# Performance work log

Measured on AMD Instinct MI355X. Metric: run time of the kernel, lower is better.

Reference implementation:

```python
import jax, jax.numpy as jnp
import numpy as np

N, E, B = 100000, 1600000, 128
ND, ED, H, NC = 91, 20, 128, 3
EPS = 1e-5


def setup_inputs() -> dict:
    key = jax.random.key(0)
    ks = jax.random.split(key, 16)
    s = 0.05
    inp = {
        "node_feats": jax.random.normal(ks[0], (N, ND), jnp.float32),
        "edge_index": jax.random.randint(ks[1], (2, E), 0, N, dtype=jnp.int32),
        "edge_feats": jax.random.normal(ks[2], (E, ED), jnp.float32),
        "batch": jnp.sort(jax.random.randint(ks[3], (N,), 0, B, dtype=jnp.int32)),
        # params
        "embed_w": jax.random.normal(ks[4], (ND, H), jnp.float32) * s,
        "embed_b": jnp.zeros((H,), jnp.float32),
        "conv_wsrc": jax.random.normal(ks[5], (NC, H, 2 * H), jnp.float32) * s,
        "conv_wdst": jax.random.normal(ks[6], (NC, H, 2 * H), jnp.float32) * s,
        "conv_we": jax.random.normal(ks[7], (NC, ED, 2 * H), jnp.float32) * s,
        "conv_b": jnp.zeros((NC, 2 * H), jnp.float32),
        "bn_gamma": jnp.ones((NC, H), jnp.float32),
        "bn_beta": jnp.zeros((NC, H), jnp.float32),
        "fc1_w": jax.random.normal(ks[8], (H, H), jnp.float32) * s,
        "fc1_b": jnp.zeros((H,), jnp.float32),
        "fc_bn_gamma": jnp.ones((H,), jnp.float32),
        "fc_bn_beta": jnp.zeros((H,), jnp.float32),
        "out_w": jax.random.normal(ks[9], (H, 1), jnp.float32) * s,
        "out_b": jnp.zeros((1,), jnp.float32),
    }
    return inp


def _bn(x, gamma, beta):
    # training-mode batchnorm over axis 0, biased variance (torch semantics)
    m = x.mean(0)
    v = x.var(0)
    return (x - m) * jax.lax.rsqrt(v + EPS) * gamma + beta


def reference(node_feats, edge_index, edge_feats, batch, embed_w, embed_b,
              conv_wsrc, conv_wdst, conv_we, conv_b, bn_gamma, bn_beta,
              fc1_w, fc1_b, fc_bn_gamma, fc_bn_beta, out_w, out_b):
    h = node_feats @ embed_w + embed_b  # (N, H)
    src, dst = edge_index[0], edge_index[1]
    for i in range(NC):
        # CGCNN gated conv: Linear on concat[h_src, h_dst, e] split into 3 matmuls
        z = (h[src] @ conv_wsrc[i] + h[dst] @ conv_wdst[i]
             + edge_feats @ conv_we[i] + conv_b[i])  # (E, 2H)
        msg = jax.nn.sigmoid(z[:, :H]) * jax.nn.softplus(z[:, H:])
        agg = jax.ops.segment_sum(msg, dst, num_segments=N)  # (N, H)
        h = jax.nn.relu(h + _bn(agg, bn_gamma[i], bn_beta[i]))
    # global mean pool over graphs
    counts = jnp.maximum(
        jax.ops.segment_sum(jnp.ones((h.shape[0], 1), h.dtype), batch, num_segments=B), 1.0)
    g = jax.ops.segment_sum(h, batch, num_segments=B) / counts  # (B, H)
    x = jax.nn.relu(_bn(g @ fc1_w + fc1_b, fc_bn_gamma, fc_bn_beta))
    return x @ out_w + out_b  # (B, 1)
```

## Files before the change

kernel.cpp:

```cpp
#include <hip/hip_runtime.h>
#include <hip/hip_bf16.h>

#define NN 100000
#define EE 1600000
#define HH 128
#define NDIM 91
#define EDIM 20
#define BB 128
#define EPSF 1e-5f
#define NBLK 4096
#define PER 400
#define ECAP (NBLK * PER)
#define LN2I 1.44269504f
#define NPART 512

typedef __attribute__((ext_vector_type(8))) short short8v;
typedef __attribute__((ext_vector_type(4))) float f32x4;

__device__ __forceinline__ short f2bs(float x) {
  __hip_bfloat16 b = __float2bfloat16(x);
  return *reinterpret_cast<short*>(&b);
}
__device__ __forceinline__ float bl(unsigned int u) {
  union { unsigned int i; float f; } x; x.i = u << 16; return x.f;
}
__device__ __forceinline__ float bh(unsigned int u) {
  union { unsigned int i; float f; } x; x.i = u & 0xffff0000u; return x.f;
}

__global__ __launch_bounds__(256) void k_embed(const float* __restrict__ nf,
                                               const float* __restrict__ W,
                                               const float* __restrict__ b,
                                               float* __restrict__ h) {
  __shared__ float w_s[NDIM * HH];
  __shared__ float b_s[HH];
  __shared__ float a_s[16 * 92];
  for (int i = threadIdx.x; i < NDIM * HH; i += 256) w_s[i] = W[i];
  if (threadIdx.x < HH) b_s[threadIdx.x] = b[threadIdx.x];
  __syncthreads();
  int col = threadIdx.x & 127, rs = threadIdx.x >> 7;
  for (int base = blockIdx.x * 16; base < NN; base += gridDim.x * 16) {
    int nrows = min(16, NN - base);
    int tot = nrows * NDIM;
    for (int i = threadIdx.x; i < tot; i += 256) {
      int r = i / NDIM;
      a_s[r * 92 + (i - r * NDIM)] = nf[(size_t)base * NDIM + i];
    }
    __syncthreads();
    float acc[8];
#pragma unroll
    for (int r = 0; r < 8; r++) acc[r] = 0.f;
    for (int k = 0; k < NDIM; k++) {
      float w = w_s[k * HH + col];
#pragma unroll
      for (int r = 0; r < 8; r++) acc[r] += a_s[(rs * 8 + r) * 92 + k] * w;
    }
#pragma unroll
    for (int r = 0; r < 8; r++) {
      int row = base + rs * 8 + r;
      if (row < NN) h[(size_t)row * HH + col] = acc[r] + b_s[col];
    }
    __syncthreads();
  }
}

__global__ __launch_bounds__(256) void k_wprep(const float* __restrict__ Wsrc,
                                               const float* __restrict__ Wdst,
                                               const float* __restrict__ We,
                                               const float* __restrict__ bias,
                                               short* __restrict__ wt,
                                               short* __restrict__ Web) {
  int i = blockIdx.x * 256 + threadIdx.x;
  if (i < 2 * 256 * 128) {
    int mat = i >> 15;
    int r = (i >> 7) & 255;
    int k = i & 127;
    const float* W = mat ? Wdst : Wsrc;
    wt[i] = f2bs(W[k * 256 + r]);
  } else if (i < 2 * 256 * 128 + 256 * 32) {
    int j = i - 2 * 256 * 128;
    int c = j >> 5, k = j & 31;
    float v = (k < EDIM) ? We[k * 256 + c] : (k == EDIM ? bias[c] : 0.f);
    float sc = (c < 128) ? -LN2I : LN2I;
    Web[j] = f2bs(v * sc);
  }
}

__global__ __launch_bounds__(256) void k_node_mm(float* __restrict__ h,
                                                 const float* __restrict__ agg,
                                                 const float* __restrict__ stats,
                                                 const short* __restrict__ wt,
                                                 unsigned int* __restrict__ hs2,
                                                 unsigned int* __restrict__ hd2,
                                                 int apply) {
  __shared__ short hlds[64 * 128];
  __shared__ float st_s[256];
  int base = blockIdx.x * 64;
  int t = threadIdx.x;
  if (apply) {
    if (t < 256) st_s[t] = stats[t];
    __syncthreads();
  }
#pragma unroll
  for (int p = 0; p < 4; p++) {
    int e0 = (p * 256 + t) * 8;
    int row = e0 >> 7, col = e0 & 127;
    int gr = base + row;
    float4 f0 = make_float4(0.f, 0.f, 0.f, 0.f), f1 = f0;
    if (gr < NN) {
      f0 = *(const float4*)&h[(size_t)gr * 128 + col];
      f1 = *(const float4*)&h[(size_t)gr * 128 + col + 4];
      if (apply) {
        float4 a0 = *(const float4*)&agg[(size_t)gr * 128 + col];
        float4 a1 = *(const float4*)&agg[(size_t)gr * 128 + col + 4];
        f0.x = fmaxf(f0.x + a0.x * st_s[col] + st_s[128 + col], 0.f);
        f0.y = fmaxf(f0.y + a0.y * st_s[col + 1] + st_s[129 + col], 0.f);
        f0.z = fmaxf(f0.z + a0.z * st_s[col + 2] + st_s[130 + col], 0.f);
        f0.w = fmaxf(f0.w + a0.w * st_s[col + 3] + st_s[131 + col], 0.f);
        f1.x = fmaxf(f1.x + a1.x * st_s[col + 4] + st_s[132 + col], 0.f);
        f1.y = fmaxf(f1.y + a1.y * st_s[col + 5] + st_s[133 + col], 0.f);
        f1.z = fmaxf(f1.z + a1.z * st_s[col + 6] + st_s[134 + col], 0.f);
        f1.w = fmaxf(f1.w + a1.w * st_s[col + 7] + st_s[135 + col], 0.f);
        *(float4*)&h[(size_t)gr * 128 + col] = f0;
        *(float4*)&h[(size_t)gr * 128 + col + 4] = f1;
      }
    }
    short8v u;
    u[0] = f2bs(f0.x); u[1] = f2bs(f0.y); u[2] = f2bs(f0.z); u[3] = f2bs(f0.w);
    u[4] = f2bs(f1.x); u[5] = f2bs(f1.y); u[6] = f2bs(f1.z); u[7] = f2bs(f1.w);
    *(short8v*)&hlds[e0] = u;
  }
  __syncthreads();
  int w = t >> 6, l = t & 63;
  int cl = l & 15, kg = l >> 4;
  short8v a[4];
#pragma unroll
  for (int kk = 0; kk < 4; kk++)
    a[kk] = *(const short8v*)&hlds[(w * 16 + cl) * 128 + kk * 32 + kg * 8];
#pragma unroll
  for (int mat = 0; mat < 2; mat++) {
    const short* wtm = wt + mat * 256 * 128;
    unsigned int* out = mat ? hd2 : hs2;
    f32x4 acc[16];
#pragma unroll
    for (int ct = 0; ct < 16; ct++) acc[ct] = (f32x4)(0.f);
#pragma unroll
    for (int ct = 0; ct < 16; ct++) {
#pragma unroll
      for (int kk = 0; kk < 4; kk++) {
        short8v b = *(const short8v*)&wtm[(ct * 16 + cl) * 128 + kk * 32 + kg * 8];
        acc[ct] = __builtin_amdgcn_mfma_f32_16x16x32_bf16(a[kk], b, acc[ct], 0, 0, 0);
      }
    }
#pragma unroll
    for (int j = 0; j < 4; j++) {
#pragma unroll
      for (int r = 0; r < 4; r++) {
        int gr = base + w * 16 + kg * 4 + r;
        if (gr < NN) {
          unsigned short g0 = (unsigned short)f2bs(-LN2I * acc[2 * j][r]);
          unsigned short s0 = (unsigned short)f2bs(LN2I * acc[2 * j + 8][r]);
          unsigned short g1 = (unsigned short)f2bs(-LN2I * acc[2 * j + 1][r]);
          unsigned short s1 = (unsigned short)f2bs(LN2I * acc[2 * j + 9][r]);
          uint2 val;
          val.x = (unsigned int)g0 | ((unsigned int)s0 << 16);
          val.y = (unsigned int)g1 | ((unsigned int)s1 << 16);
          *(uint2*)&out[(size_t)gr * 128 + j * 32 + (cl << 1)] = val;
        }
      }
    }
  }
}

__global__ __launch_bounds__(256) void k_hist(const int* __restrict__ dst,
                                              int* __restrict__ cnt) {
  for (int e = blockIdx.x * 256 + threadIdx.x; e < EE; e += gridDim.x * 256)
    atomicAdd(&cnt[dst[e]], 1);
}

__global__ __launch_bounds__(1024) void k_scan(const int* __restrict__ cnt,
                                               int* __restrict__ off) {
  __shared__ int ps[1024];
  int t = threadIdx.x;
  const int R = (NN + 1023) / 1024;
  int b0 = t * R, b1 = min(NN, b0 + R);
  int s = 0;
  for (int i = b0; i < b1; i++) s += cnt[i];
  ps[t] = s;
  __syncthreads();
  for (int d = 1; d < 1024; d <<= 1) {
    int v = (t >= d) ? ps[t - d] : 0;
    __syncthreads();
    ps[t] += v;
    __syncthreads();
  }
  int run = (t == 0) ? 0 : ps[t - 1];
  for (int i = b0; i < b1; i++) {
    off[i] = run;
    run += cnt[i];
  }
}

__global__ __launch_bounds__(256) void k_scatter(const int* __restrict__ src,
                                                 const int* __restrict__ dst,
                                                 const float* __restrict__ ef,
                                                 int* __restrict__ off,
                                                 int* __restrict__ src_s,
                                                 int* __restrict__ dst_s,
                                                 short* __restrict__ efp) {
  for (int e = blockIdx.x * 256 + threadIdx.x; e < EE; e += gridDim.x * 256) {
    int d = dst[e];
    int pos = atomicAdd(&off[d], 1);
    src_s[pos] = src[e];
    dst_s[pos] = d;
    const float4* in = (const float4*)&ef[(size_t)e * EDIM];
    float4 q0 = in[0], q1 = in[1], q2 = in[2], q3 = in[3], q4 = in[4];
    short8v u0, u1, u2, u3;
    u0[0] = f2bs(q0.x); u0[1] = f2bs(q0.y); u0[2] = f2bs(q0.z); u0[3] = f2bs(q0.w);
    u0[4] = f2bs(q1.x); u0[5] = f2bs(q1.y); u0[6] = f2bs(q1.z); u0[7] = f2bs(q1.w);
    u1[0] = f2bs(q2.x); u1[1] = f2bs(q2.y); u1[2] = f2bs(q2.z); u1[3] = f2bs(q2.w);
    u1[4] = f2bs(q3.x); u1[5] = f2bs(q3.y); u1[6] = f2bs(q3.z); u1[7] = f2bs(q3.w);
    u2[0] = f2bs(q4.x); u2[1] = f2bs(q4.y); u2[2] = f2bs(q4.z); u2[3] = f2bs(q4.w);
    u2[4] = f2bs(1.0f); u2[5] = 0; u2[6] = 0; u2[7] = 0;
    u3 = (short8v)(short)0;
    short8v* op = (short8v*)&efp[(size_t)pos * 32];
    op[0] = u0; op[1] = u1; op[2] = u2; op[3] = u3;
  }
}

__global__ __launch_bounds__(256) void k_padtail(int* __restrict__ src_s,
                                                 int* __restrict__ dst_s,
                                                 short* __restrict__ efp) {
  int e = EE + blockIdx.x * 256 + threadIdx.x;
  if (e >= ECAP) return;
  src_s[e] = 0;
  dst_s[e] = -2;
  short8v z = (short8v)(short)0;
  short8v* op = (short8v*)&efp[(size_t)e * 32];
  op[0] = z; op[1] = z; op[2] = z; op[3] = z;
}

__global__ __launch_bounds__(256) void k_edge_v8(
    const unsigned int* __restrict__ hs2, const unsigned int* __restrict__ hd2,
    const short* __restrict__ efp, const int* __restrict__ srcp,
    const int* __restrict__ dstp, const short* __restrict__ Web,
    float* __restrict__ agg) {
  const int i0 = blockIdx.x * PER;
  int t = threadIdx.x;
  int w = t >> 6, l = t & 63, cl = l & 15, kg = l >> 4;
  int c0 = w * 32 + cl, c1 = c0 + 16;
  int pairoff = w * 32 + (cl << 1);
  short8v bg0 = *(const short8v*)&Web[c0 * 32 + kg * 8];
  short8v bg1 = *(const short8v*)&Web[c1 * 32 + kg * 8];
  short8v bs0 = *(const short8v*)&Web[(128 + c0) * 32 + kg * 8];
  short8v bs1 = *(const short8v*)&Web[(128 + c1) * 32 + kg * 8];
  int cur = -1;
  float acc0 = 0.f, acc1 = 0.f;
  float hg0 = 0.f, hp0 = 0.f, hg1 = 0.f, hp1 = 0.f;
  const int o_a_base = i0 + (cl >> 2) * 100 + (cl & 3);
  const int o_e_base = i0 + kg * 100;
  for (int it = 0; it < 25; ++it) {
    int off4 = it * 4;
    short8v a = *(const short8v*)&efp[(size_t)(o_a_base + off4) * 32 + kg * 8];
    f32x4 zgv0 = __builtin_amdgcn_mfma_f32_16x16x32_bf16(a, bg0, (f32x4)(0.f), 0, 0, 0);
    f32x4 zgv1 = __builtin_amdgcn_mfma_f32_16x16x32_bf16(a, bg1, (f32x4)(0.f), 0, 0, 0);
    f32x4 zsv0 = __builtin_amdgcn_mfma_f32_16x16x32_bf16(a, bs0, (f32x4)(0.f), 0, 0, 0);
    f32x4 zsv1 = __builtin_amdgcn_mfma_f32_16x16x32_bf16(a, bs1, (f32x4)(0.f), 0, 0, 0);
    int o_e = o_e_base + off4;
    int4 s4 = *(const int4*)&srcp[o_e];
    int4 d4 = *(const int4*)&dstp[o_e];
    int ss[4] = {s4.x, s4.y, s4.z, s4.w};
    int dd[4] = {d4.x, d4.y, d4.z, d4.w};
    uint2 us[4], xs[4];
#pragma unroll
    for (int r = 0; r < 4; ++r) {
      us[r] = *(const uint2*)&hs2[((size_t)ss[r] << 7) + pairoff];
      int dc = dd[r] < 0 ? 0 : dd[r];
      xs[r] = *(const uint2*)&hd2[((size_t)dc << 7) + pairoff];
    }
#pragma unroll
    for (int r = 0; r < 4; ++r) {
      int d = dd[r];
      bool nw = (d != cur);
      if (nw && cur >= 0) {
        atomicAdd(&agg[cur * HH + c0], acc0);
        atomicAdd(&agg[cur * HH + c1], acc1);
      }
      acc0 = nw ? 0.f : acc0;
      acc1 = nw ? 0.f : acc1;
      hg0 = nw ? bl(xs[r].x) : hg0;
      hp0 = nw ? bh(xs[r].x) : hp0;
      hg1 = nw ? bl(xs[r].y) : hg1;
      hp1 = nw ? bh(xs[r].y) : hp1;
      cur = d;
      float zgN0 = zgv0[r] + bl(us[r].x) + hg0;
      float zsp0 = zsv0[r] + bh(us[r].x) + hp0;
      float zgN1 = zgv1[r] + bl(us[r].y) + hg1;
      float zsp1 = zsv1[r] + bh(us[r].y) + hp1;
      float sp0 = __builtin_amdgcn_logf(1.f + __builtin_amdgcn_exp2f(zsp0));
      float sp1 = __builtin_amdgcn_logf(1.f + __builtin_amdgcn_exp2f(zsp1));
      acc0 += sp0 * __builtin_amdgcn_rcpf(1.f + __builtin_amdgcn_exp2f(zgN0));
      acc1 += sp1 * __builtin_amdgcn_rcpf(1.f + __builtin_amdgcn_exp2f(zgN1));
    }
  }
  if (cur >= 0) {
    atomicAdd(&agg[cur * HH + c0], acc0);
    atomicAdd(&agg[cur * HH + c1], acc1);
  }
}

__global__ __launch_bounds__(256) void k_bn_stats(const float* __restrict__ agg,
                                                  float* __restrict__ part) {
  int col = threadIdx.x & 127, hlf = threadIdx.x >> 7;
  float s = 0.f, sq = 0.f;
  for (int row = blockIdx.x * 2 + hlf; row < NN; row += NPART * 2) {
    float v = agg[(size_t)row * HH + col];
    s += v; sq += v * v;
  }
  __shared__ float ls[256], lq[256];
  ls[threadIdx.x] = s; lq[threadIdx.x] = sq;
  __syncthreads();
  if (hlf == 0) {
    part[(size_t)blockIdx.x * 256 + col] = ls[col] + ls[col + 128];
    part[(size_t)blockIdx.x * 256 + 128 + col] = lq[col] + lq[col + 128];
  }
}

__global__ void k_bn_fin(const float* __restrict__ part, float* __restrict__ stats,
                         const float* __restrict__ gam, const float* __restrict__ bet) {
  int c = threadIdx.x;
  if (c >= HH) return;
  float s = 0.f, q = 0.f;
  for (int b = 0; b < NPART; b++) {
    s += part[(size_t)b * 256 + c];
    q += part[(size_t)b * 256 + 128 + c];
  }
  float mean = s / (float)NN;
  float var = q / (float)NN - mean * mean;
  float sc = rsqrtf(var + EPSF) * gam[c];
  stats[c] = sc;
  stats[HH + c] = bet[c] - mean * sc;
}

__global__ void k_pool(const float* __restrict__ h, const float* __restrict__ agg,
                       const float* __restrict__ stats, const int* __restrict__ batch,
                       float* __restrict__ g, float* __restrict__ gcnt) {
  int col = threadIdx.x;
  float sc = stats[col], sh = stats[128 + col];
  int chunk = (NN + gridDim.x - 1) / gridDim.x;
  int n0 = blockIdx.x * chunk, n1 = min(NN, n0 + chunk);
  if (n0 >= n1) return;
  int cur = batch[n0];
  float acc = 0.f, cnt = 0.f;
  for (int n = n0; n < n1; n++) {
    int bb = batch[n];
    if (bb != cur) {
      atomicAdd(&g[cur * HH + col], acc);
      if (col == 0) atomicAdd(&gcnt[cur], cnt);
      acc = 0.f; cnt = 0.f; cur = bb;
    }
    acc += fmaxf(h[(size_t)n * HH + col] + agg[(size_t)n * HH + col] * sc + sh, 0.f);
    cnt += 1.f;
  }
  atomicAdd(&g[cur * HH + col], acc);
  if (col == 0) atomicAdd(&gcnt[cur], cnt);
}

__global__ __launch_bounds__(256) void k_final(float* __restrict__ g,
                                               const float* __restrict__ gcnt,
                                               const float* __restrict__ fc1w,
                                               const float* __restrict__ fc1b,
                                               const float* __restrict__ gam,
                                               const float* __restrict__ bet,
                                               const float* __restrict__ ow,
                                               const float* __restrict__ ob,
                                               float* __restrict__ out) {
  __shared__ float w_s[HH * HH];
  __shared__ float y_s[BB * HH];
  __shared__ float ls[256], lq[256];
  for (int i = threadIdx.x; i < HH * HH; i += 256) w_s[i] = fc1w[i];
  for (int i = threadIdx.x; i < BB * HH; i += 256) {
    int r = i >> 7;
    g[i] = g[i] / fmaxf(gcnt[r], 1.f);
  }
  __syncthreads();
  int c = threadIdx.x & 127, h2 = threadIdx.x >> 7;
  for (int rr = 0; rr < 64; rr++) {
    int r = h2 * 64 + rr;
    float acc = fc1b[c];
    for (int k = 0; k < HH; k++) acc += g[r * HH + k] * w_s[k * HH + c];
    y_s[r * HH + c] = acc;
  }
  __syncthreads();
  float s = 0.f, sq = 0.f;
  for (int rr = 0; rr < 64; rr++) {
    float v = y_s[(h2 * 64 + rr) * HH + c];
    s += v; sq += v * v;
  }
  ls[threadIdx.x] = s; lq[threadIdx.x] = sq;
  __syncthreads();
  if (h2 == 0) {
    float ss = ls[c] + ls[c + 128], qq = lq[c] + lq[c + 128];
    float mean = ss / (float)BB, var = qq / (float)BB - mean * mean;
    float sc = rsqrtf(var + EPSF) * gam[c];
    ls[c] = sc;
    lq[c] = bet[c] - mean * sc;
  }
  __syncthreads();
  for (int rr = 0; rr < 64; rr++) {
    int r = h2 * 64 + rr;
    y_s[r * HH + c] = fmaxf(y_s[r * HH + c] * ls[c] + lq[c], 0.f);
  }
  __syncthreads();
  int r2 = threadIdx.x >> 1, hf = threadIdx.x & 1;
  float acc = 0.f;
  for (int k = hf * 64; k < hf * 64 + 64; k++) acc += y_s[r2 * HH + k] * ow[k];
  __syncthreads();
  ls[threadIdx.x] = acc;
  __syncthreads();
  if (hf == 0) out[r2] = ls[threadIdx.x] + ls[threadIdx.x + 1] + ob[0];
}

extern "C" void kernel_launch(void* const* d_in, const int* in_sizes, int n_in,
                              void* d_out, int out_size, void* d_ws, size_t ws_size,
                              hipStream_t stream) {
  (void)in_sizes; (void)n_in; (void)out_size; (void)ws_size;
  const float* node_feats = (const float*)d_in[0];
  const int* edge_index = (const int*)d_in[1];
  const float* edge_feats = (const float*)d_in[2];
  const int* batch = (const int*)d_in[3];
  const float* embed_w = (const float*)d_in[4];
  const float* embed_b = (const float*)d_in[5];
  const float* conv_wsrc = (const float*)d_in[6];
  const float* conv_wdst = (const float*)d_in[7];
  const float* conv_we = (const float*)d_in[8];
  const float* conv_b = (const float*)d_in[9];
  const float* bn_gamma = (const float*)d_in[10];
  const float* bn_beta = (const float*)d_in[11];
  const float* fc1_w = (const float*)d_in[12];
  const float* fc1_b = (const float*)d_in[13];
  const float* fc_bn_gamma = (const float*)d_in[14];
  const float* fc_bn_beta = (const float*)d_in[15];
  const float* out_w = (const float*)d_in[16];
  const float* out_b = (const float*)d_in[17];

  char* ws = (char*)d_ws;
  size_t o = 0;
  float* h = (float*)(ws + o);              o += (size_t)NN * HH * 4;
  unsigned int* hs2 = (unsigned int*)(ws + o); o += (size_t)NN * 128 * 4;
  unsigned int* hd2 = (unsigned int*)(ws + o); o += (size_t)NN * 128 * 4;
  float* agg = (float*)(ws + o);            o += (size_t)NN * HH * 4;
  short* efp = (short*)(ws + o);            o += (size_t)ECAP * 32 * 2;
  int* src_s = (int*)(ws + o);              o += (size_t)ECAP * 4;
  int* dst_s = (int*)(ws + o);              o += (size_t)ECAP * 4;
  int* cnt = (int*)(ws + o);                o += (size_t)NN * 4;
  int* off = (int*)(ws + o);                o += (size_t)NN * 4;
  short* wt = (short*)(ws + o);             o += (size_t)2 * 256 * 128 * 2;
  short* Web = (short*)(ws + o);            o += (size_t)256 * 32 * 2;
  float* part = (float*)(ws + o);           o += (size_t)NPART * 256 * 4;
  float* stats = (float*)(ws + o);          o += 256 * 4;
  float* g = (float*)(ws + o);              o += (size_t)BB * HH * 4;
  float* gcnt = (float*)(ws + o);           o += BB * 4;

  const int* src = edge_index;
  const int* dst = edge_index + EE;

  hipMemsetAsync(cnt, 0, (size_t)NN * 4, stream);
  k_hist<<<2048, 256, 0, stream>>>(dst, cnt);
  k_scan<<<1, 1024, 0, stream>>>(cnt, off);
  k_scatter<<<2048, 256, 0, stream>>>(src, dst, edge_feats, off, src_s, dst_s, efp);
  k_padtail<<<(ECAP - EE + 255) / 256, 256, 0, stream>>>(src_s, dst_s, efp);

  k_embed<<<512, 256, 0, stream>>>(node_feats, embed_w, embed_b, h);

  for (int i = 0; i < 3; i++) {
    k_wprep<<<288, 256, 0, stream>>>(conv_wsrc + (size_t)i * HH * 256,
                                     conv_wdst + (size_t)i * HH * 256,
                                     conv_we + (size_t)i * EDIM * 256,
                                     conv_b + (size_t)i * 256, wt, Web);
    k_node_mm<<<(NN + 63) / 64, 256, 0, stream>>>(h, agg, stats, wt, hs2, hd2,
                                                  i > 0 ? 1 : 0);
    hipMemsetAsync(agg, 0, (size_t)NN * HH * 4, stream);
    k_edge_v8<<<NBLK, 256, 0, stream>>>(hs2, hd2, efp, src_s, dst_s, Web, agg);
    k_bn_stats<<<NPART, 256, 0, stream>>>(agg, part);
    k_bn_fin<<<1, 128, 0, stream>>>(part, stats, bn_gamma + i * HH, bn_beta + i * HH);
  }

  hipMemsetAsync(g, 0, (size_t)BB * HH * 4, stream);
  hipMemsetAsync(gcnt, 0, BB * 4, stream);
  k_pool<<<1024, 128, 0, stream>>>(h, agg, stats, batch, g, gcnt);
  k_final<<<1, 256, 0, stream>>>(g, gcnt, fc1_w, fc1_b, fc_bn_gamma, fc_bn_beta,
                                 out_w, out_b, (float*)d_out);
}
```

Baseline: 1.823 ms.

## Fold memsets, padding and weight prep into existing kernels to cut launches

Weight conversion for all three conv layers now runs once in a single kernel, which also zeroes the histogram counts. The agg buffer is zeroed inside the node matmul kernel, the tail padding is merged into the scatter kernel, and the pooling buffers are cleared in the last BN finalize kernel. Together these remove several separate memsets and launches per forward pass. The edge kernel also drops the per-segment carried dst terms in favour of per-edge values and requests higher occupancy, which may change register pressure.

```diff
diff --git a/kernel.cpp b/kernel.cpp
--- a/kernel.cpp
+++ b/kernel.cpp
@@ -64,30 +64,37 @@
   }
 }
 
-__global__ __launch_bounds__(256) void k_wprep(const float* __restrict__ Wsrc,
-                                               const float* __restrict__ Wdst,
-                                               const float* __restrict__ We,
-                                               const float* __restrict__ bias,
-                                               short* __restrict__ wt,
-                                               short* __restrict__ Web) {
+__global__ __launch_bounds__(256) void k_wprep3(const float* __restrict__ conv_wsrc,
+                                                const float* __restrict__ conv_wdst,
+                                                const float* __restrict__ conv_we,
+                                                const float* __restrict__ conv_b,
+                                                short* __restrict__ wt3,
+                                                short* __restrict__ Web3,
+                                                int* __restrict__ cnt) {
   int i = blockIdx.x * 256 + threadIdx.x;
-  if (i < 2 * 256 * 128) {
-    int mat = i >> 15;
-    int r = (i >> 7) & 255;
-    int k = i & 127;
-    const float* W = mat ? Wdst : Wsrc;
-    wt[i] = f2bs(W[k * 256 + r]);
-  } else if (i < 2 * 256 * 128 + 256 * 32) {
-    int j = i - 2 * 256 * 128;
-    int c = j >> 5, k = j & 31;
+  if (i < NN) cnt[i] = 0;
+  if (i >= 3 * 73728) return;
+  int layer = i / 73728;
+  int j = i - layer * 73728;
+  if (j < 65536) {
+    int mat = j >> 15;
+    int r = (j >> 7) & 255;
+    int k = j & 127;
+    const float* W = (mat ? conv_wdst : conv_wsrc) + (size_t)layer * HH * 256;
+    wt3[(size_t)layer * 65536 + j] = f2bs(W[k * 256 + r]);
+  } else {
+    int jj = j - 65536;
+    int c = jj >> 5, k = jj & 31;
+    const float* We = conv_we + (size_t)layer * EDIM * 256;
+    const float* bias = conv_b + (size_t)layer * 256;
     float v = (k < EDIM) ? We[k * 256 + c] : (k == EDIM ? bias[c] : 0.f);
     float sc = (c < 128) ? -LN2I : LN2I;
-    Web[j] = f2bs(v * sc);
+    Web3[(size_t)layer * 8192 + jj] = f2bs(v * sc);
   }
 }
 
 __global__ __launch_bounds__(256) void k_node_mm(float* __restrict__ h,
-                                                 const float* __restrict__ agg,
+                                                 float* __restrict__ agg,
                                                  const float* __restrict__ stats,
                                                  const short* __restrict__ wt,
                                                  unsigned int* __restrict__ hs2,
@@ -101,12 +108,13 @@
     if (t < 256) st_s[t] = stats[t];
     __syncthreads();
   }
+  const float4 z4 = make_float4(0.f, 0.f, 0.f, 0.f);
 #pragma unroll
   for (int p = 0; p < 4; p++) {
     int e0 = (p * 256 + t) * 8;
     int row = e0 >> 7, col = e0 & 127;
     int gr = base + row;
-    float4 f0 = make_float4(0.f, 0.f, 0.f, 0.f), f1 = f0;
+    float4 f0 = z4, f1 = z4;
     if (gr < NN) {
       f0 = *(const float4*)&h[(size_t)gr * 128 + col];
       f1 = *(const float4*)&h[(size_t)gr * 128 + col + 4];
@@ -124,6 +132,8 @@
         *(float4*)&h[(size_t)gr * 128 + col] = f0;
         *(float4*)&h[(size_t)gr * 128 + col + 4] = f1;
       }
+      *(float4*)&agg[(size_t)gr * 128 + col] = z4;
+      *(float4*)&agg[(size_t)gr * 128 + col + 4] = z4;
     }
     short8v u;
     u[0] = f2bs(f0.x); u[1] = f2bs(f0.y); u[2] = f2bs(f0.z); u[3] = f2bs(f0.w);
@@ -133,6 +143,7 @@
   __syncthreads();
   int w = t >> 6, l = t & 63;
   int cl = l & 15, kg = l >> 4;
+  bool full = (base + 64 <= NN);
   short8v a[4];
 #pragma unroll
   for (int kk = 0; kk < 4; kk++)
@@ -157,7 +168,7 @@
 #pragma unroll
       for (int r = 0; r < 4; r++) {
         int gr = base + w * 16 + kg * 4 + r;
-        if (gr < NN) {
+        if (full || gr < NN) {
           unsigned short g0 = (unsigned short)f2bs(-LN2I * acc[2 * j][r]);
           unsigned short s0 = (unsigned short)f2bs(LN2I * acc[2 * j + 8][r]);
           unsigned short g1 = (unsigned short)f2bs(-LN2I * acc[2 * j + 1][r]);
@@ -208,39 +219,35 @@
                                                  int* __restrict__ src_s,
                                                  int* __restrict__ dst_s,
                                                  short* __restrict__ efp) {
-  for (int e = blockIdx.x * 256 + threadIdx.x; e < EE; e += gridDim.x * 256) {
-    int d = dst[e];
-    int pos = atomicAdd(&off[d], 1);
-    src_s[pos] = src[e];
-    dst_s[pos] = d;
-    const float4* in = (const float4*)&ef[(size_t)e * EDIM];
-    float4 q0 = in[0], q1 = in[1], q2 = in[2], q3 = in[3], q4 = in[4];
-    short8v u0, u1, u2, u3;
-    u0[0] = f2bs(q0.x); u0[1] = f2bs(q0.y); u0[2] = f2bs(q0.z); u0[3] = f2bs(q0.w);
-    u0[4] = f2bs(q1.x); u0[5] = f2bs(q1.y); u0[6] = f2bs(q1.z); u0[7] = f2bs(q1.w);
-    u1[0] = f2bs(q2.x); u1[1] = f2bs(q2.y); u1[2] = f2bs(q2.z); u1[3] = f2bs(q2.w);
-    u1[4] = f2bs(q3.x); u1[5] = f2bs(q3.y); u1[6] = f2bs(q3.z); u1[7] = f2bs(q3.w);
-    u2[0] = f2bs(q4.x); u2[1] = f2bs(q4.y); u2[2] = f2bs(q4.z); u2[3] = f2bs(q4.w);
-    u2[4] = f2bs(1.0f); u2[5] = 0; u2[6] = 0; u2[7] = 0;
-    u3 = (short8v)(short)0;
-    short8v* op = (short8v*)&efp[(size_t)pos * 32];
-    op[0] = u0; op[1] = u1; op[2] = u2; op[3] = u3;
-  }
-}
-
-__global__ __launch_bounds__(256) void k_padtail(int* __restrict__ src_s,
-                                                 int* __restrict__ dst_s,
-                                                 short* __restrict__ efp) {
-  int e = EE + blockIdx.x * 256 + threadIdx.x;
-  if (e >= ECAP) return;
-  src_s[e] = 0;
-  dst_s[e] = -2;
-  short8v z = (short8v)(short)0;
-  short8v* op = (short8v*)&efp[(size_t)e * 32];
-  op[0] = z; op[1] = z; op[2] = z; op[3] = z;
-}
-
-__global__ __launch_bounds__(256) void k_edge_v8(
+  for (int e = blockIdx.x * 256 + threadIdx.x; e < ECAP; e += gridDim.x * 256) {
+    if (e < EE) {
+      int d = dst[e];
+      int pos = atomicAdd(&off[d], 1);
+      src_s[pos] = src[e];
+      dst_s[pos] = d;
+      const float4* in = (const float4*)&ef[(size_t)e * EDIM];
+      float4 q0 = in[0], q1 = in[1], q2 = in[2], q3 = in[3], q4 = in[4];
+      short8v u0, u1, u2, u3;
+      u0[0] = f2bs(q0.x); u0[1] = f2bs(q0.y); u0[2] = f2bs(q0.z); u0[3] = f2bs(q0.w);
+      u0[4] = f2bs(q1.x); u0[5] = f2bs(q1.y); u0[6] = f2bs(q1.z); u0[7] = f2bs(q1.w);
+      u1[0] = f2bs(q2.x); u1[1] = f2bs(q2.y); u1[2] = f2bs(q2.z); u1[3] = f2bs(q2.w);
+      u1[4] = f2bs(q3.x); u1[5] = f2bs(q3.y); u1[6] = f2bs(q3.z); u1[7] = f2bs(q3.w);
+      u2[0] = f2bs(q4.x); u2[1] = f2bs(q4.y); u2[2] = f2bs(q4.z); u2[3] = f2bs(q4.w);
+      u2[4] = f2bs(1.0f); u2[5] = 0; u2[6] = 0; u2[7] = 0;
+      u3 = (short8v)(short)0;
+      short8v* op = (short8v*)&efp[(size_t)pos * 32];
+      op[0] = u0; op[1] = u1; op[2] = u2; op[3] = u3;
+    } else {
+      src_s[e] = 0;
+      dst_s[e] = -2;
+      short8v z = (short8v)(short)0;
+      short8v* op = (short8v*)&efp[(size_t)e * 32];
+      op[0] = z; op[1] = z; op[2] = z; op[3] = z;
+    }
+  }
+}
+
+__global__ __launch_bounds__(256, 8) void k_edge_v9(
     const unsigned int* __restrict__ hs2, const unsigned int* __restrict__ hd2,
     const short* __restrict__ efp, const int* __restrict__ srcp,
     const int* __restrict__ dstp, const short* __restrict__ Web,
@@ -256,7 +263,6 @@
   short8v bs1 = *(const short8v*)&Web[(128 + c1) * 32 + kg * 8];
   int cur = -1;
   float acc0 = 0.f, acc1 = 0.f;
-  float hg0 = 0.f, hp0 = 0.f, hg1 = 0.f, hp1 = 0.f;
   const int o_a_base = i0 + (cl >> 2) * 100 + (cl & 3);
   const int o_e_base = i0 + kg * 100;
   for (int it = 0; it < 25; ++it) {
@@ -288,15 +294,11 @@
       }
       acc0 = nw ? 0.f : acc0;
       acc1 = nw ? 0.f : acc1;
-      hg0 = nw ? bl(xs[r].x) : hg0;
-      hp0 = nw ? bh(xs[r].x) : hp0;
-      hg1 = nw ? bl(xs[r].y) : hg1;
-      hp1 = nw ? bh(xs[r].y) : hp1;
       cur = d;
-      float zgN0 = zgv0[r] + bl(us[r].x) + hg0;
-      float zsp0 = zsv0[r] + bh(us[r].x) + hp0;
-      float zgN1 = zgv1[r] + bl(us[r].y) + hg1;
-      float zsp1 = zsv1[r] + bh(us[r].y) + hp1;
+      float zgN0 = zgv0[r] + bl(us[r].x) + bl(xs[r].x);
+      float zsp0 = zsv0[r] + bh(us[r].x) + bh(xs[r].x);
+      float zgN1 = zgv1[r] + bl(us[r].y) + bl(xs[r].y);
+      float zsp1 = zsv1[r] + bh(us[r].y) + bh(xs[r].y);
       float sp0 = __builtin_amdgcn_logf(1.f + __builtin_amdgcn_exp2f(zsp0));
       float sp1 = __builtin_amdgcn_logf(1.f + __builtin_amdgcn_exp2f(zsp1));
       acc0 += sp0 * __builtin_amdgcn_rcpf(1.f + __builtin_amdgcn_exp2f(zgN0));
@@ -326,20 +328,30 @@
   }
 }
 
-__global__ void k_bn_fin(const float* __restrict__ part, float* __restrict__ stats,
-                         const float* __restrict__ gam, const float* __restrict__ bet) {
+__global__ __launch_bounds__(256) void k_bn_fin(const float* __restrict__ part,
+                                                float* __restrict__ stats,
+                                                const float* __restrict__ gam,
+                                                const float* __restrict__ bet,
+                                                float* __restrict__ g,
+                                                float* __restrict__ gcnt,
+                                                int zero_g) {
   int c = threadIdx.x;
-  if (c >= HH) return;
-  float s = 0.f, q = 0.f;
-  for (int b = 0; b < NPART; b++) {
-    s += part[(size_t)b * 256 + c];
-    q += part[(size_t)b * 256 + 128 + c];
-  }
-  float mean = s / (float)NN;
-  float var = q / (float)NN - mean * mean;
-  float sc = rsqrtf(var + EPSF) * gam[c];
-  stats[c] = sc;
-  stats[HH + c] = bet[c] - mean * sc;
+  if (c < HH) {
+    float s = 0.f, q = 0.f;
+    for (int b = 0; b < NPART; b++) {
+      s += part[(size_t)b * 256 + c];
+      q += part[(size_t)b * 256 + 128 + c];
+    }
+    float mean = s / (float)NN;
+    float var = q / (float)NN - mean * mean;
+    float sc = rsqrtf(var + EPSF) * gam[c];
+    stats[c] = sc;
+    stats[HH + c] = bet[c] - mean * sc;
+  }
+  if (zero_g) {
+    for (int i = threadIdx.x; i < BB * HH; i += 256) g[i] = 0.f;
+    if (threadIdx.x < BB) gcnt[threadIdx.x] = 0.f;
+  }
 }
 
 __global__ void k_pool(const float* __restrict__ h, const float* __restrict__ agg,
@@ -455,8 +467,8 @@
   int* dst_s = (int*)(ws + o);              o += (size_t)ECAP * 4;
   int* cnt = (int*)(ws + o);                o += (size_t)NN * 4;
   int* off = (int*)(ws + o);                o += (size_t)NN * 4;
-  short* wt = (short*)(ws + o);             o += (size_t)2 * 256 * 128 * 2;
-  short* Web = (short*)(ws + o);            o += (size_t)256 * 32 * 2;
+  short* wt3 = (short*)(ws + o);            o += (size_t)3 * 2 * 256 * 128 * 2;
+  short* Web3 = (short*)(ws + o);           o += (size_t)3 * 256 * 32 * 2;
   float* part = (float*)(ws + o);           o += (size_t)NPART * 256 * 4;
   float* stats = (float*)(ws + o);          o += 256 * 4;
   float* g = (float*)(ws + o);              o += (size_t)BB * HH * 4;
@@ -465,29 +477,25 @@
   const int* src = edge_index;
   const int* dst = edge_index + EE;
 
-  hipMemsetAsync(cnt, 0, (size_t)NN * 4, stream);
+  k_wprep3<<<(3 * 73728 + 255) / 256, 256, 0, stream>>>(conv_wsrc, conv_wdst,
+                                                        conv_we, conv_b, wt3, Web3, cnt);
   k_hist<<<2048, 256, 0, stream>>>(dst, cnt);
   k_scan<<<1, 1024, 0, stream>>>(cnt, off);
   k_scatter<<<2048, 256, 0, stream>>>(src, dst, edge_feats, off, src_s, dst_s, efp);
-  k_padtail<<<(ECAP - EE + 255) / 256, 256, 0, stream>>>(src_s, dst_s, efp);
 
   k_embed<<<512, 256, 0, stream>>>(node_feats, embed_w, embed_b, h);
 
   for (int i = 0; i < 3; i++) {
-    k_wprep<<<288, 256, 0, stream>>>(conv_wsrc + (size_t)i * HH * 256,
-                                     conv_wdst + (size_t)i * HH * 256,
-                                     conv_we + (size_t)i * EDIM * 256,
-                                     conv_b + (size_t)i * 256, wt, Web);
-    k_node_mm<<<(NN + 63) / 64, 256, 0, stream>>>(h, agg, stats, wt, hs2, hd2,
-                                                  i > 0 ? 1 : 0);
-    hipMemsetAsync(agg, 0, (size_t)NN * HH * 4, stream);
-    k_edge_v8<<<NBLK, 256, 0, stream>>>(hs2, hd2, efp, src_s, dst_s, Web, agg);
+    k_node_mm<<<(NN + 63) / 64, 256, 0, stream>>>(h, agg, stats,
+                                                  wt3 + (size_t)i * 65536,
+                                                  hs2, hd2, i > 0 ? 1 : 0);
+    k_edge_v9<<<NBLK, 256, 0, stream>>>(hs2, hd2, efp, src_s, dst_s,
+                                        Web3 + (size_t)i * 8192, agg);
     k_bn_stats<<<NPART, 256, 0, stream>>>(agg, part);
-    k_bn_fin<<<1, 128, 0, stream>>>(part, stats, bn_gamma + i * HH, bn_beta + i * HH);
-  }
-
-  hipMemsetAsync(g, 0, (size_t)BB * HH * 4, stream);
-  hipMemsetAsync(gcnt, 0, BB * 4, stream);
+    k_bn_fin<<<1, 256, 0, stream>>>(part, stats, bn_gamma + i * HH,
+                                    bn_beta + i * HH, g, gcnt, i == 2 ? 1 : 0);
+  }
+
   k_pool<<<1024, 128, 0, stream>>>(h, agg, stats, batch, g, gcnt);
   k_final<<<1, 256, 0, stream>>>(g, gcnt, fc1_w, fc1_b, fc_bn_gamma, fc_bn_beta,
                                  out_w, out_b, (float*)d_out);
```

New measurement: 1.933 ms. 6.1% more time.
